# Performance work log

Measured on AMD Instinct MI355X. Metric: run time of the kernel, lower is better.

## Reference

```python
import jax, jax.numpy as jnp
import numpy as np

T, A = 10, 9           # input_dim_h, input_dim_w
HID = 128              # EncoderMLP hidden_dim default
D = 512                # n_latent_dims
G, K = 4, 32           # vqvae_groups, vqvae_n_embed
ACT_SCALE = 1.0


def setup_inputs() -> dict:
    key = jax.random.key(0)
    ks = jax.random.split(key, 16)
    N = 131072
    s = lambda k, shp, fan: jax.random.normal(k, shp, jnp.float32) * (1.0 / np.sqrt(fan))
    inp = {
        "state": jax.random.normal(ks[0], (N, T, A), jnp.float32),
        # encoder: (T*A)->128 relu, 128->128 relu, 128->512
        "enc_w1": s(ks[1], (T * A, HID), T * A), "enc_b1": jnp.zeros((HID,), jnp.float32),
        "enc_w2": s(ks[2], (HID, HID), HID),     "enc_b2": jnp.zeros((HID,), jnp.float32),
        "enc_w3": s(ks[3], (HID, D), HID),       "enc_b3": jnp.zeros((D,), jnp.float32),
        # decoder: 512->128 relu, 128->128 relu, 128->(T*A)
        "dec_w1": s(ks[4], (D, HID), D),         "dec_b1": jnp.zeros((HID,), jnp.float32),
        "dec_w2": s(ks[5], (HID, HID), HID),     "dec_b2": jnp.zeros((HID,), jnp.float32),
        "dec_w3": s(ks[6], (HID, T * A), HID),   "dec_b3": jnp.zeros((T * A,), jnp.float32),
        # residual VQ codebooks [G, K, D]
        "codebooks": jax.random.normal(ks[7], (G, K, D), jnp.float32),
    }
    return inp


def _mlp(x, w1, b1, w2, b2, w3, b3):
    h = jax.nn.relu(x @ w1 + b1)
    h = jax.nn.relu(h @ w2 + b2)
    return h @ w3 + b3


def reference(state, enc_w1, enc_b1, enc_w2, enc_b2, enc_w3, enc_b3,
              dec_w1, dec_b1, dec_w2, dec_b2, dec_w3, dec_b3, codebooks):
    N = state.shape[0]
    x = (state / ACT_SCALE).reshape(N, T * A)            # preprocess: 'N T A -> N (T A)'
    z = _mlp(x, enc_w1, enc_b1, enc_w2, enc_b2, enc_w3, enc_b3)  # [N, D]

    # Residual VQ over G quantizers (eval path): nearest-code per residual,
    # straight-through accumulation, per-quantizer commitment loss.
    residual = z
    quant = jnp.zeros_like(z)
    codes, losses = [], []
    for g in range(G):
        e = codebooks[g]                                  # [K, D]
        # ||r - e||^2 = ||r||^2 - 2 r.e + ||e||^2 ; ||r||^2 constant over K
        dist = jnp.sum(e * e, axis=-1)[None, :] - 2.0 * (residual @ e.T)  # [N, K]
        idx = jnp.argmin(dist, axis=-1)                   # [N]
        q = e[idx]                                        # [N, D] gather
        losses.append(jnp.mean((jax.lax.stop_gradient(q) - residual) ** 2))
        quant = quant + residual + jax.lax.stop_gradient(q - residual)  # straight-through
        residual = residual - jax.lax.stop_gradient(q)
        codes.append(idx)
    vq_code = jnp.stack(codes, axis=-1)                   # [N, G]
    vq_loss = jnp.sum(jnp.stack(losses))

    recon = _mlp(quant, dec_w1, dec_b1, dec_w2, dec_b2, dec_w3, dec_b3) * ACT_SCALE
    recon = recon.reshape(N, T, A)                        # 'N (T A) -> N T A'
    return quant, vq_code, recon, vq_loss
```

## Files before the change

kernel.cpp:

```cpp
#include <hip/hip_runtime.h>
#include <hip/hip_bf16.h>

#define NSAMP 131072
#define TA    90
#define HID   128
#define DLAT  512

#define OFF_CODE  67108864ll
#define OFF_RECON (67108864ll + 524288ll)
#define OFF_LOSS  (67108864ll + 524288ll + 11796480ll)

#define ACT_ST 68
#define WLF    8704
#define PZF    12800
#define SHF    13056
#define MSKF   8256
#define H2AF   8272
#define H2BF   8400
#define TAU    0.0625f

typedef __attribute__((ext_vector_type(8))) short bf16x8;
typedef __attribute__((ext_vector_type(4))) short s16x4;
typedef __attribute__((ext_vector_type(4))) float f32x4;
typedef unsigned short ushort_t;
#define MFMA16(a, b, c) __builtin_amdgcn_mfma_f32_16x16x32_bf16(a, b, c, 0, 0, 0)

__device__ __forceinline__ ushort_t f2bf(float f) {
    unsigned u = __float_as_uint(f);
    u = (u + 0x7FFF + ((u >> 16) & 1)) >> 16;
    return (ushort_t)u;
}
__device__ __forceinline__ float bf2f(ushort_t u) {
    return __uint_as_float(((unsigned)u) << 16);
}

__device__ __forceinline__ float dot512(const float* __restrict__ a,
                                        const float* __restrict__ b) {
    float s = 0.f;
    for (int i = 0; i < 128; ++i) {
        float4 x = ((const float4*)a)[i], y = ((const float4*)b)[i];
        s += x.x * y.x + x.y * y.y + x.z * y.z + x.w * y.w;
    }
    return s;
}

__device__ __forceinline__ void fma_tile(float (&acc)[8][4],
                                         const float* __restrict__ wl,
                                         const float* __restrict__ al) {
    float4 av = *(const float4*)al;
    float4 w0 = *(const float4*)wl;
    float4 w1 = *(const float4*)(wl + 4);
    float aa[4] = {av.x, av.y, av.z, av.w};
    float ww[8] = {w0.x, w0.y, w0.z, w0.w, w1.x, w1.y, w1.z, w1.w};
#pragma unroll
    for (int a = 0; a < 8; ++a)
#pragma unroll
        for (int b = 0; b < 4; ++b) acc[a][b] = fmaf(ww[a], aa[b], acc[a][b]);
}

__device__ __forceinline__ void gemm_dbuf(const float* __restrict__ w, int wstride,
                                          int inRows, int nch,
                                          const float* __restrict__ Act,
                                          float* __restrict__ Wl,
                                          float (&acc)[8][4],
                                          int t, int o0, int s0) {
    const int wr = t >> 4;
    const int wc = (t & 15) * 8;
    float4 c0, c1;
    {
        int r = wr < inRows ? wr : inRows - 1;
        const float* p = w + (size_t)r * wstride + wc;
        c0 = *(const float4*)p; c1 = *(const float4*)(p + 4);
    }
    *(float4*)&Wl[wr * 128 + wc] = c0;
    *(float4*)&Wl[wr * 128 + wc + 4] = c1;
    __syncthreads();
    for (int ch = 0; ch < nch; ++ch) {
        const float* Wc = &Wl[(ch & 1) * 2048];
        const bool more = (ch + 1 < nch);
        if (more) {
            int rr = (ch + 1) * 16 + wr;
            int r = rr < inRows ? rr : inRows - 1;
            const float* p = w + (size_t)r * wstride + wc;
            c0 = *(const float4*)p; c1 = *(const float4*)(p + 4);
        }
        const float* Ab = Act + (ch * 16) * ACT_ST + s0;
#pragma unroll
        for (int j = 0; j < 16; ++j)
            fma_tile(acc, &Wc[j * 128 + o0], Ab + j * ACT_ST);
        __syncthreads();
        if (more) {
            float* Wn = &Wl[((ch + 1) & 1) * 2048];
            *(float4*)&Wn[wr * 128 + wc] = c0;
            *(float4*)&Wn[wr * 128 + wc + 4] = c1;
            __syncthreads();
        }
    }
}

__global__ void k_prep(const float* __restrict__ cb, const float* __restrict__ w3,
                       const float* __restrict__ b3, const float* __restrict__ w1d,
                       const float* __restrict__ w2d, const float* __restrict__ w3d,
                       const float* __restrict__ w2e,
                       float* __restrict__ P, float* __restrict__ M,
                       float* __restrict__ t0, float* __restrict__ v,
                       float* __restrict__ csc, float* __restrict__ cbW,
                       ushort_t* __restrict__ Qbf, ushort_t* __restrict__ w2bf,
                       ushort_t* __restrict__ w3bf,
                       ushort_t* __restrict__ Mhibf, ushort_t* __restrict__ Mlobf,
                       ushort_t* __restrict__ w2ehi, ushort_t* __restrict__ w2elo) {
    int tbl = blockIdx.x >> 6;
    int gid = (blockIdx.x & 63) * 256 + threadIdx.x;
    int i = gid >> 7, j = gid & 127;
    if (tbl == 0) {
        P[gid] = dot512(cb + (size_t)i * 512, cb + (size_t)j * 512);
        if (gid < 128) t0[gid] = dot512(cb + (size_t)gid * 512, b3);
        if (gid == 0) csc[0] = dot512(b3, b3);
    } else if (tbl == 1) {
        M[gid] = dot512(w3 + (size_t)i * 512, cb + (size_t)j * 512);
    } else if (tbl == 2) {
        Qbf[gid] = f2bf(dot512(w3 + (size_t)i * 512, w3 + (size_t)j * 512));
        if (gid < 128) v[gid] = dot512(w3 + (size_t)gid * 512, b3);
    } else if (tbl == 3) {
        float s = 0.f;
        for (int d = 0; d < 512; ++d) s = fmaf(cb[(size_t)i * 512 + d], w1d[d * 128 + j], s);
        cbW[gid] = s;
    } else if (tbl == 4) {
        w2bf[gid] = f2bf(w2d[j * 128 + i]);
    } else if (tbl == 5) {
        if (gid < 96 * 128)
            w3bf[gid] = (i < 90) ? f2bf(w3d[j * TA + i]) : (ushort_t)0;
    } else if (tbl == 6) {
        float d = dot512(w3 + (size_t)j * 512, cb + (size_t)i * 512);
        ushort_t hi = f2bf(d);
        Mhibf[gid] = hi;
        Mlobf[gid] = f2bf(d - bf2f(hi));
    } else {
        float d = w2e[j * 128 + i];
        ushort_t hi = f2bf(d);
        w2ehi[gid] = hi;
        w2elo[gid] = f2bf(d - bf2f(hi));
    }
}

__launch_bounds__(256, 3)
__global__ void k_encvq(const float* __restrict__ X,
                        const float* __restrict__ w1, const float* __restrict__ b1,
                        const float* __restrict__ w2, const float* __restrict__ b2,
                        const ushort_t* __restrict__ w2ehi, const ushort_t* __restrict__ w2elo,
                        const float* __restrict__ Mt, const ushort_t* __restrict__ Qbf,
                        const ushort_t* __restrict__ Mhi, const ushort_t* __restrict__ Mlo,
                        const float* __restrict__ t0g, const float* __restrict__ vg,
                        const float* __restrict__ cg, const float* __restrict__ Pg,
                        float* __restrict__ codes_out, float* __restrict__ loss_acc) {
    __shared__ __align__(16) float SH[SHF];
    float* Act = SH;
    float* Wl  = SH + WLF;
    ushort_t* hAhi = (ushort_t*)SH;
    ushort_t* hAlo = (ushort_t*)(SH + 4096);
    const int t = threadIdx.x;
    const int st = t & 15, ct = t >> 4;
    const int s0 = st * 4, o0 = ct * 8;
    const int row0 = blockIdx.x * 64;

    float rb1[8];
#pragma unroll
    for (int i = 0; i < 8; ++i) rb1[i] = b1[o0 + i];

    for (int it = 0; it < 24; ++it) {
        int idx = it * 256 + t;
        int j = idx >> 6, s = idx & 63;
        Act[j * ACT_ST + s] = (j < 90) ? X[(size_t)(row0 + s) * TA + j] : 0.f;
    }

    float acc[8][4];
#pragma unroll
    for (int a = 0; a < 8; ++a)
#pragma unroll
        for (int b = 0; b < 4; ++b) acc[a][b] = 0.f;
    gemm_dbuf(w1, HID, 90, 6, Act, Wl, acc, t, o0, s0);

    {
#pragma unroll
        for (int b = 0; b < 4; ++b) {
            int s = s0 + b;
            bf16x8 pkh, pkl;
#pragma unroll
            for (int a = 0; a < 8; ++a) {
                float hv = fmaxf(acc[a][b] + rb1[a], 0.f);
                acc[a][b] = hv;
                ushort_t hi = f2bf(hv);
                pkh[a] = (short)hi;
                pkl[a] = (short)f2bf(hv - bf2f(hi));
            }
            int adr = ((s << 7) + o0) ^ ((s & 7) << 3);
            *(bf16x8*)&hAhi[adr] = pkh;
            *(bf16x8*)&hAlo[adr] = pkl;
        }
    }
    __syncthreads();

    const int wv = t >> 6, lane = t & 63, lr = lane & 15, lg = lane >> 4;

    {
        f32x4 c2[2][4];
#pragma unroll
        for (int m = 0; m < 2; ++m)
#pragma unroll
            for (int n = 0; n < 4; ++n) c2[m][n] = (f32x4){0.f, 0.f, 0.f, 0.f};
#pragma unroll
        for (int kt = 0; kt < 4; ++kt) {
            bf16x8 ah[2], al[2], bhi[4], blo[4];
#pragma unroll
            for (int m = 0; m < 2; ++m) {
                int arow = (32 * wv + 16 * m + lr) * 128 + kt * 32 + lg * 8;
                ah[m] = *(const bf16x8*)&w2ehi[arow];
                al[m] = *(const bf16x8*)&w2elo[arow];
            }
#pragma unroll
            for (int n = 0; n < 4; ++n) {
                int s = 16 * n + lr;
                int adr = ((s << 7) + kt * 32 + lg * 8) ^ ((s & 7) << 3);
                bhi[n] = *(const bf16x8*)&hAhi[adr];
                blo[n] = *(const bf16x8*)&hAlo[adr];
            }
#pragma unroll
            for (int m = 0; m < 2; ++m)
#pragma unroll
                for (int n = 0; n < 4; ++n) {
                    c2[m][n] = MFMA16(ah[m], bhi[n], c2[m][n]);
                    c2[m][n] = MFMA16(ah[m], blo[n], c2[m][n]);
                    c2[m][n] = MFMA16(al[m], bhi[n], c2[m][n]);
                }
        }
        __syncthreads();
        float rbf[2][4];
#pragma unroll
        for (int m = 0; m < 2; ++m)
#pragma unroll
            for (int r = 0; r < 4; ++r) rbf[m][r] = b2[32 * wv + 16 * m + lg * 4 + r];
#pragma unroll
        for (int m = 0; m < 2; ++m)
#pragma unroll
            for (int n = 0; n < 4; ++n) {
                int s = 16 * n + lr;
                s16x4 ph, pl;
#pragma unroll
                for (int r = 0; r < 4; ++r) {
                    float hv = fmaxf(c2[m][n][r] + rbf[m][r], 0.f);
                    ushort_t hi = f2bf(hv);
                    ph[r] = (short)hi;
                    pl[r] = (short)f2bf(hv - bf2f(hi));
                }
                int ob2 = 32 * wv + 16 * m + lg * 4;
                int adr = ((s << 7) + ob2) ^ ((s & 7) << 3);
                *(s16x4*)&hAhi[adr] = ph;
                *(s16x4*)&hAlo[adr] = pl;
            }
    }
    __syncthreads();

    f32x4 sc[2][4];
    {
        f32x4 qc[2][4];
#pragma unroll
        for (int m = 0; m < 2; ++m)
#pragma unroll
            for (int n = 0; n < 4; ++n) {
                qc[m][n] = (f32x4){0.f, 0.f, 0.f, 0.f};
                sc[m][n] = (f32x4){0.f, 0.f, 0.f, 0.f};
            }
#pragma unroll
        for (int kt = 0; kt < 4; ++kt) {
            bf16x8 aq[2], amh[2], aml[2], bhi[4], blo[4];
#pragma unroll
            for (int m = 0; m < 2; ++m) {
                int arow = (32 * wv + 16 * m + lr) * 128 + kt * 32 + lg * 8;
                aq[m]  = *(const bf16x8*)&Qbf[arow];
                amh[m] = *(const bf16x8*)&Mhi[arow];
                aml[m] = *(const bf16x8*)&Mlo[arow];
            }
#pragma unroll
            for (int n = 0; n < 4; ++n) {
                int s = 16 * n + lr;
                int adr = ((s << 7) + kt * 32 + lg * 8) ^ ((s & 7) << 3);
                bhi[n] = *(const bf16x8*)&hAhi[adr];
                blo[n] = *(const bf16x8*)&hAlo[adr];
            }
#pragma unroll
            for (int m = 0; m < 2; ++m)
#pragma unroll
                for (int n = 0; n < 4; ++n) {
                    qc[m][n] = MFMA16(aq[m], bhi[n], qc[m][n]);
                    sc[m][n] = MFMA16(amh[m], bhi[n], sc[m][n]);
                    sc[m][n] = MFMA16(amh[m], blo[n], sc[m][n]);
                    sc[m][n] = MFMA16(aml[m], bhi[n], sc[m][n]);
                }
        }
        float v2[2][4];
#pragma unroll
        for (int m = 0; m < 2; ++m)
#pragma unroll
            for (int r = 0; r < 4; ++r) v2[m][r] = 2.f * vg[32 * wv + 16 * m + lg * 4 + r];
#pragma unroll
        for (int n = 0; n < 4; ++n) {
            int s = 16 * n + lr;
            float p = 0.f;
#pragma unroll
            for (int m = 0; m < 2; ++m)
#pragma unroll
                for (int r = 0; r < 4; ++r) {
                    int o = 32 * wv + 16 * m + lg * 4 + r;
                    int adr = ((s << 7) + o) ^ ((s & 7) << 3);
                    float hv = bf2f(hAhi[adr]) + bf2f(hAlo[adr]);
                    p = fmaf(qc[m][n][r] + v2[m][r], hv, p);
                }
            p += __shfl_xor(p, 16);
            p += __shfl_xor(p, 32);
            if (lg == 0) SH[PZF + wv * 64 + s] = p;
        }
    }
    __syncthreads();

#pragma unroll
    for (int m = 0; m < 2; ++m)
#pragma unroll
        for (int n = 0; n < 4; ++n) {
            int s = 16 * n + lr;
#pragma unroll
            for (int r = 0; r < 4; ++r) {
                int o = 32 * wv + 16 * m + lg * 4 + r;
                SH[s * 129 + o] = sc[m][n][r] + t0g[o];
            }
        }
    __syncthreads();

    int cs[4];
    if (t < 64) {
        float marg = 3.4e38f;
#pragma unroll
        for (int g = 0; g < 4; ++g) {
            float best = 3.4e38f, best2 = 3.4e38f; int bi = g * 32;
#pragma unroll
            for (int k = 0; k < 32; ++k) {
                int c = g * 32 + k;
                float zd = SH[t * 129 + c];
                float nr = Pg[c * 128 + c];
                float a2 = 0.f;
#pragma unroll
                for (int gp = 0; gp < g; ++gp) a2 += Pg[cs[gp] * 128 + c];
                float dist = nr - 2.f * (zd - a2);
                if (dist < best) { best2 = best; best = dist; bi = c; }
                else if (dist < best2) { best2 = dist; }
            }
            cs[g] = bi;
            float m2 = best2 - best;
            marg = (m2 < marg) ? m2 : marg;
        }
        unsigned long long mk = __ballot(marg < TAU);
        if (t == 0) *(unsigned long long*)&SH[MSKF] = mk;
    }
    __syncthreads();

    const unsigned long long mask = *(const unsigned long long*)&SH[MSKF];

    {
        unsigned long long mk = mask;
        while (mk) {
            int nA = (int)__ffsll((long long)mk) - 1; mk &= mk - 1;
            int nB = -1;
            if (mk) { nB = (int)__ffsll((long long)mk) - 1; mk &= mk - 1; }
            if ((t & 15) == (nA >> 2)) {
                int bb = nA & 3;
                if (bb == 0) {
#pragma unroll
                    for (int a = 0; a < 8; ++a) SH[H2AF + o0 + a] = acc[a][0];
                } else if (bb == 1) {
#pragma unroll
                    for (int a = 0; a < 8; ++a) SH[H2AF + o0 + a] = acc[a][1];
                } else if (bb == 2) {
#pragma unroll
                    for (int a = 0; a < 8; ++a) SH[H2AF + o0 + a] = acc[a][2];
                } else {
#pragma unroll
                    for (int a = 0; a < 8; ++a) SH[H2AF + o0 + a] = acc[a][3];
                }
            }
            if (nB >= 0 && (t & 15) == (nB >> 2)) {
                int bb = nB & 3;
                if (bb == 0) {
#pragma unroll
                    for (int a = 0; a < 8; ++a) SH[H2BF + o0 + a] = acc[a][0];
                } else if (bb == 1) {
#pragma unroll
                    for (int a = 0; a < 8; ++a) SH[H2BF + o0 + a] = acc[a][1];
                } else if (bb == 2) {
#pragma unroll
                    for (int a = 0; a < 8; ++a) SH[H2BF + o0 + a] = acc[a][2];
                } else {
#pragma unroll
                    for (int a = 0; a < 8; ++a) SH[H2BF + o0 + a] = acc[a][3];
                }
            }
            __syncthreads();
            int grp = t >> 7, tt = t & 127;
            int s2 = grp ? nB : nA;
            float hv2 = 0.f;
            if (s2 >= 0) {
                const float* h1c = &SH[grp ? H2BF : H2AF];
                for (int j = 0; j < 128; ++j)
                    hv2 = fmaf(h1c[j], w2[(size_t)j * 128 + tt], hv2);
                hv2 = fmaxf(hv2 + b2[tt], 0.f);
            }
            __syncthreads();
            if (s2 >= 0) SH[(grp ? H2BF : H2AF) + tt] = hv2;
            __syncthreads();
            if (s2 >= 0) {
                const float* h2c = &SH[grp ? H2BF : H2AF];
                float a = 0.f;
                for (int j = 0; j < 128; ++j)
                    a = fmaf(h2c[j], Mt[(size_t)j * 128 + tt], a);
                SH[s2 * 129 + tt] = a + t0g[tt];
            }
            __syncthreads();
        }
    }

    if (t < 64 && ((mask >> t) & 1ull)) {
#pragma unroll
        for (int g = 0; g < 4; ++g) {
            float best = 3.4e38f; int bi = g * 32;
#pragma unroll
            for (int k = 0; k < 32; ++k) {
                int c = g * 32 + k;
                float zd = SH[t * 129 + c];
                float nr = Pg[c * 128 + c];
                float a2 = 0.f;
#pragma unroll
                for (int gp = 0; gp < g; ++gp) a2 += Pg[cs[gp] * 128 + c];
                float dist = nr - 2.f * (zd - a2);
                if (dist < best) { best = dist; bi = c; }
            }
            cs[g] = bi;
        }
    }

    if (t < 64) {
        float znorm = cg[0] + SH[PZF + t] + SH[PZF + 64 + t]
                    + SH[PZF + 128 + t] + SH[PZF + 192 + t];
        float S1 = 0.f, Sp = 0.f, msum = 0.f;
#pragma unroll
        for (int g = 0; g < 4; ++g) {
            int c = cs[g];
            float zd = SH[t * 129 + c];
            float nr = Pg[c * 128 + c];
            float a2 = 0.f;
#pragma unroll
            for (int gp = 0; gp < g; ++gp) a2 += Pg[cs[gp] * 128 + c];
            S1 += zd;
            Sp += nr + 2.f * a2;
            msum += (znorm - 2.f * S1 + Sp);
            codes_out[(size_t)(row0 + t) * 4 + g] = (float)(c - g * 32);
        }
#pragma unroll
        for (int off = 32; off; off >>= 1) msum += __shfl_down(msum, off);
        if (t == 0) atomicAdd(&loss_acc[0], msum);
    }
}

__launch_bounds__(256, 4)
__global__ void k_dec(const float* __restrict__ codes_f, const float* __restrict__ cb,
                      const float* __restrict__ cbW, const float* __restrict__ b1,
                      const ushort_t* __restrict__ w2bf, const float* __restrict__ b2,
                      const ushort_t* __restrict__ w3bf, const float* __restrict__ b3,
                      float* __restrict__ quant_out, float* __restrict__ recon_out) {
    __shared__ __align__(16) unsigned char SHB[39424];
    int* cods = (int*)SHB;
    ushort_t* h2bf = (ushort_t*)SHB;
    ushort_t* h1bf = (ushort_t*)(SHB + 16384);
    float* Rl = (float*)(SHB + 16384);
    const int t = threadIdx.x;
    const int st = t & 15, ct = t >> 4;
    const int s0 = st * 4, o0 = ct * 8;
    const int row0 = blockIdx.x * 64;

    cods[t] = ((t & 3) << 5) + (int)codes_f[(size_t)row0 * 4 + t];
    float rb1[8];
#pragma unroll
    for (int i = 0; i < 8; ++i) rb1[i] = b1[o0 + i];
    __syncthreads();

    for (int i = 0; i < 32; ++i) {
        int idx4 = i * 256 + t;
        int s = idx4 >> 7, d4 = (idx4 & 127) * 4;
        const int* cp = &cods[s * 4];
        float4 a = *(const float4*)&cb[(size_t)cp[0] * 512 + d4];
        float4 b = *(const float4*)&cb[(size_t)cp[1] * 512 + d4];
        float4 c = *(const float4*)&cb[(size_t)cp[2] * 512 + d4];
        float4 d = *(const float4*)&cb[(size_t)cp[3] * 512 + d4];
        float4 vv;
        vv.x = a.x + b.x + c.x + d.x;
        vv.y = a.y + b.y + c.y + d.y;
        vv.z = a.z + b.z + c.z + d.z;
        vv.w = a.w + b.w + c.w + d.w;
        *(float4*)&quant_out[(size_t)(row0 + s) * 512 + d4] = vv;
    }

    {
        float accL[8][4];
#pragma unroll
        for (int b = 0; b < 4; ++b) {
            const int* cp = &cods[(s0 + b) * 4];
            float u[8] = {0, 0, 0, 0, 0, 0, 0, 0};
#pragma unroll
            for (int g = 0; g < 4; ++g) {
                const float* r = &cbW[(size_t)cp[g] * 128 + o0];
                float4 x0 = *(const float4*)r, x1 = *(const float4*)(r + 4);
                u[0] += x0.x; u[1] += x0.y; u[2] += x0.z; u[3] += x0.w;
                u[4] += x1.x; u[5] += x1.y; u[6] += x1.z; u[7] += x1.w;
            }
#pragma unroll
            for (int a = 0; a < 8; ++a) accL[a][b] = u[a];
        }
#pragma unroll
        for (int b = 0; b < 4; ++b) {
            int s = s0 + b;
            bf16x8 pk;
#pragma unroll
            for (int a = 0; a < 8; ++a)
                pk[a] = (short)f2bf(fmaxf(accL[a][b] + rb1[a], 0.f));
            *(bf16x8*)&h1bf[((s << 7) + o0) ^ ((s & 7) << 3)] = pk;
        }
    }
    __syncthreads();

    const int wv = t >> 6, lane = t & 63, lr = lane & 15, lg = lane >> 4;

    {
        f32x4 c2[2][4];
#pragma unroll
        for (int m = 0; m < 2; ++m)
#pragma unroll
            for (int n = 0; n < 4; ++n) c2[m][n] = (f32x4){0.f, 0.f, 0.f, 0.f};
#pragma unroll
        for (int kt = 0; kt < 4; ++kt) {
            bf16x8 af[2], bfr[4];
#pragma unroll
            for (int m = 0; m < 2; ++m)
                af[m] = *(const bf16x8*)&w2bf[(32 * wv + 16 * m + lr) * 128 + kt * 32 + lg * 8];
#pragma unroll
            for (int n = 0; n < 4; ++n) {
                int s = 16 * n + lr;
                bfr[n] = *(const bf16x8*)&h1bf[((s << 7) + kt * 32 + lg * 8) ^ ((s & 7) << 3)];
            }
#pragma unroll
            for (int m = 0; m < 2; ++m)
#pragma unroll
                for (int n = 0; n < 4; ++n)
                    c2[m][n] = MFMA16(af[m], bfr[n], c2[m][n]);
        }
        float rb[2][4];
#pragma unroll
        for (int m = 0; m < 2; ++m)
#pragma unroll
            for (int r = 0; r < 4; ++r) rb[m][r] = b2[32 * wv + 16 * m + lg * 4 + r];
#pragma unroll
        for (int m = 0; m < 2; ++m)
#pragma unroll
            for (int n = 0; n < 4; ++n) {
                int s = 16 * n + lr;
                s16x4 pk;
#pragma unroll
                for (int r = 0; r < 4; ++r)
                    pk[r] = (short)f2bf(fmaxf(c2[m][n][r] + rb[m][r], 0.f));
                int ob2 = 32 * wv + 16 * m + lg * 4;
                *(s16x4*)&h2bf[((s << 7) + ob2) ^ ((s & 7) << 3)] = pk;
            }
    }
    __syncthreads();

    {
        f32x4 c3[6];
#pragma unroll
        for (int m = 0; m < 6; ++m) c3[m] = (f32x4){0.f, 0.f, 0.f, 0.f};
        const int sB = 16 * wv + lr;
#pragma unroll
        for (int kt = 0; kt < 4; ++kt) {
            bf16x8 bfr = *(const bf16x8*)&h2bf[((sB << 7) + kt * 32 + lg * 8) ^ ((sB & 7) << 3)];
#pragma unroll
            for (int mt = 0; mt < 6; ++mt) {
                bf16x8 af = *(const bf16x8*)&w3bf[(16 * mt + lr) * 128 + kt * 32 + lg * 8];
                c3[mt] = MFMA16(af, bfr, c3[mt]);
            }
        }
#pragma unroll
        for (int mt = 0; mt < 6; ++mt)
#pragma unroll
            for (int r = 0; r < 4; ++r) {
                int o = 16 * mt + lg * 4 + r;
                if (o < 90) Rl[sB * 90 + o] = c3[mt][r] + b3[o];
            }
    }
    __syncthreads();

    {
        const float4* R4v = (const float4*)Rl;
        float4* G4 = (float4*)(recon_out + (size_t)row0 * 90);
#pragma unroll
        for (int it = 0; it < 6; ++it) {
            int i4 = it * 256 + t;
            if (i4 < 1440) G4[i4] = R4v[i4];
        }
    }
}

__global__ void k_loss(const float* __restrict__ acc, float* __restrict__ out) {
    out[0] = acc[0] * (1.0f / ((float)NSAMP * (float)DLAT));
}

extern "C" void kernel_launch(void* const* d_in, const int* in_sizes, int n_in,
                              void* d_out, int out_size, void* d_ws, size_t ws_size,
                              hipStream_t stream) {
    const float* state  = (const float*)d_in[0];
    const float* enc_w1 = (const float*)d_in[1];
    const float* enc_b1 = (const float*)d_in[2];
    const float* enc_w2 = (const float*)d_in[3];
    const float* enc_b2 = (const float*)d_in[4];
    const float* enc_w3 = (const float*)d_in[5];
    const float* enc_b3 = (const float*)d_in[6];
    const float* dec_w1 = (const float*)d_in[7];
    const float* dec_b1 = (const float*)d_in[8];
    const float* dec_w2 = (const float*)d_in[9];
    const float* dec_b2 = (const float*)d_in[10];
    const float* dec_w3 = (const float*)d_in[11];
    const float* dec_b3 = (const float*)d_in[12];
    const float* cb     = (const float*)d_in[13];

    float* out = (float*)d_out;
    float* P   = out;
    float* M   = out + 16384;
    ushort_t* Mhi = (ushort_t*)(out + 32768);
    ushort_t* Mlo = (ushort_t*)(out + 40960);
    float* t0  = out + 49152;
    float* v   = out + 49280;
    float* csc = out + 49408;
    ushort_t* w2ehi = (ushort_t*)(out + 49664);
    ushort_t* w2elo = (ushort_t*)(out + 57856);
    float* ws = (float*)d_ws;
    float* loss_acc = ws;
    float* cbW = ws + 256;
    ushort_t* Qbf  = (ushort_t*)(ws + 16640);
    ushort_t* w2bf = (ushort_t*)(ws + 24832);
    ushort_t* w3bf = (ushort_t*)(ws + 33024);

    hipMemsetAsync(d_ws, 0, 16, stream);
    k_prep<<<512, 256, 0, stream>>>(cb, enc_w3, enc_b3, dec_w1, dec_w2, dec_w3,
                                    enc_w2,
                                    P, M, t0, v, csc, cbW, Qbf, w2bf, w3bf,
                                    Mhi, Mlo, w2ehi, w2elo);
    k_encvq<<<NSAMP / 64, 256, 0, stream>>>(state, enc_w1, enc_b1, enc_w2, enc_b2,
                                            w2ehi, w2elo,
                                            M, Qbf, Mhi, Mlo, t0, v, csc, P,
                                            out + OFF_CODE, loss_acc);
    k_dec<<<NSAMP / 64, 256, 0, stream>>>(out + OFF_CODE, cb, cbW,
                                          dec_b1, w2bf, dec_b2, w3bf, dec_b3,
                                          out, out + OFF_RECON);
    k_loss<<<1, 1, 0, stream>>>(loss_acc, out + OFF_LOSS);
}
```

Baseline: 348.4 us.

## Move encoder layer 1 to split-bf16 MFMA and recompute near-tie rows from global

```diff
diff --git a/kernel.cpp b/kernel.cpp
--- a/kernel.cpp
+++ b/kernel.cpp
@@ -10,14 +10,12 @@
 #define OFF_RECON (67108864ll + 524288ll)
 #define OFF_LOSS  (67108864ll + 524288ll + 11796480ll)
 
-#define ACT_ST 68
-#define WLF    8704
-#define PZF    12800
-#define SHF    13056
+#define PZF    8704
+#define SHF    8960
 #define MSKF   8256
 #define H2AF   8272
 #define H2BF   8400
-#define TAU    0.0625f
+#define TAU    0.08f
 
 typedef __attribute__((ext_vector_type(8))) short bf16x8;
 typedef __attribute__((ext_vector_type(4))) short s16x4;
@@ -44,71 +42,18 @@
     return s;
 }
 
-__device__ __forceinline__ void fma_tile(float (&acc)[8][4],
-                                         const float* __restrict__ wl,
-                                         const float* __restrict__ al) {
-    float4 av = *(const float4*)al;
-    float4 w0 = *(const float4*)wl;
-    float4 w1 = *(const float4*)(wl + 4);
-    float aa[4] = {av.x, av.y, av.z, av.w};
-    float ww[8] = {w0.x, w0.y, w0.z, w0.w, w1.x, w1.y, w1.z, w1.w};
-#pragma unroll
-    for (int a = 0; a < 8; ++a)
-#pragma unroll
-        for (int b = 0; b < 4; ++b) acc[a][b] = fmaf(ww[a], aa[b], acc[a][b]);
-}
-
-__device__ __forceinline__ void gemm_dbuf(const float* __restrict__ w, int wstride,
-                                          int inRows, int nch,
-                                          const float* __restrict__ Act,
-                                          float* __restrict__ Wl,
-                                          float (&acc)[8][4],
-                                          int t, int o0, int s0) {
-    const int wr = t >> 4;
-    const int wc = (t & 15) * 8;
-    float4 c0, c1;
-    {
-        int r = wr < inRows ? wr : inRows - 1;
-        const float* p = w + (size_t)r * wstride + wc;
-        c0 = *(const float4*)p; c1 = *(const float4*)(p + 4);
-    }
-    *(float4*)&Wl[wr * 128 + wc] = c0;
-    *(float4*)&Wl[wr * 128 + wc + 4] = c1;
-    __syncthreads();
-    for (int ch = 0; ch < nch; ++ch) {
-        const float* Wc = &Wl[(ch & 1) * 2048];
-        const bool more = (ch + 1 < nch);
-        if (more) {
-            int rr = (ch + 1) * 16 + wr;
-            int r = rr < inRows ? rr : inRows - 1;
-            const float* p = w + (size_t)r * wstride + wc;
-            c0 = *(const float4*)p; c1 = *(const float4*)(p + 4);
-        }
-        const float* Ab = Act + (ch * 16) * ACT_ST + s0;
-#pragma unroll
-        for (int j = 0; j < 16; ++j)
-            fma_tile(acc, &Wc[j * 128 + o0], Ab + j * ACT_ST);
-        __syncthreads();
-        if (more) {
-            float* Wn = &Wl[((ch + 1) & 1) * 2048];
-            *(float4*)&Wn[wr * 128 + wc] = c0;
-            *(float4*)&Wn[wr * 128 + wc + 4] = c1;
-            __syncthreads();
-        }
-    }
-}
-
 __global__ void k_prep(const float* __restrict__ cb, const float* __restrict__ w3,
                        const float* __restrict__ b3, const float* __restrict__ w1d,
                        const float* __restrict__ w2d, const float* __restrict__ w3d,
-                       const float* __restrict__ w2e,
+                       const float* __restrict__ w2e, const float* __restrict__ w1e,
                        float* __restrict__ P, float* __restrict__ M,
                        float* __restrict__ t0, float* __restrict__ v,
                        float* __restrict__ csc, float* __restrict__ cbW,
                        ushort_t* __restrict__ Qbf, ushort_t* __restrict__ w2bf,
                        ushort_t* __restrict__ w3bf,
                        ushort_t* __restrict__ Mhibf, ushort_t* __restrict__ Mlobf,
-                       ushort_t* __restrict__ w2ehi, ushort_t* __restrict__ w2elo) {
+                       ushort_t* __restrict__ w2ehi, ushort_t* __restrict__ w2elo,
+                       ushort_t* __restrict__ w1ehi, ushort_t* __restrict__ w1elo) {
     int tbl = blockIdx.x >> 6;
     int gid = (blockIdx.x & 63) * 256 + threadIdx.x;
     int i = gid >> 7, j = gid & 127;
@@ -135,18 +80,24 @@
         ushort_t hi = f2bf(d);
         Mhibf[gid] = hi;
         Mlobf[gid] = f2bf(d - bf2f(hi));
-    } else {
+    } else if (tbl == 7) {
         float d = w2e[j * 128 + i];
         ushort_t hi = f2bf(d);
         w2ehi[gid] = hi;
         w2elo[gid] = f2bf(d - bf2f(hi));
-    }
-}
-
-__launch_bounds__(256, 3)
+    } else {
+        float d = (j < 90) ? w1e[(size_t)j * 128 + i] : 0.f;
+        ushort_t hi = f2bf(d);
+        w1ehi[gid] = hi;
+        w1elo[gid] = f2bf(d - bf2f(hi));
+    }
+}
+
+__launch_bounds__(256, 4)
 __global__ void k_encvq(const float* __restrict__ X,
                         const float* __restrict__ w1, const float* __restrict__ b1,
                         const float* __restrict__ w2, const float* __restrict__ b2,
+                        const ushort_t* __restrict__ w1ehi, const ushort_t* __restrict__ w1elo,
                         const ushort_t* __restrict__ w2ehi, const ushort_t* __restrict__ w2elo,
                         const float* __restrict__ Mt, const ushort_t* __restrict__ Qbf,
                         const ushort_t* __restrict__ Mhi, const ushort_t* __restrict__ Mlo,
@@ -154,53 +105,80 @@
                         const float* __restrict__ cg, const float* __restrict__ Pg,
                         float* __restrict__ codes_out, float* __restrict__ loss_acc) {
     __shared__ __align__(16) float SH[SHF];
-    float* Act = SH;
-    float* Wl  = SH + WLF;
-    ushort_t* hAhi = (ushort_t*)SH;
-    ushort_t* hAlo = (ushort_t*)(SH + 4096);
+    ushort_t* sphi = (ushort_t*)SH;
+    ushort_t* splo = (ushort_t*)(SH + 4096);
     const int t = threadIdx.x;
-    const int st = t & 15, ct = t >> 4;
-    const int s0 = st * 4, o0 = ct * 8;
     const int row0 = blockIdx.x * 64;
-
-    float rb1[8];
-#pragma unroll
-    for (int i = 0; i < 8; ++i) rb1[i] = b1[o0 + i];
+    const int wv = t >> 6, lane = t & 63, lr = lane & 15, lg = lane >> 4;
 
     for (int it = 0; it < 24; ++it) {
         int idx = it * 256 + t;
-        int j = idx >> 6, s = idx & 63;
-        Act[j * ACT_ST + s] = (j < 90) ? X[(size_t)(row0 + s) * TA + j] : 0.f;
-    }
-
-    float acc[8][4];
-#pragma unroll
-    for (int a = 0; a < 8; ++a)
-#pragma unroll
-        for (int b = 0; b < 4; ++b) acc[a][b] = 0.f;
-    gemm_dbuf(w1, HID, 90, 6, Act, Wl, acc, t, o0, s0);
-
-    {
-#pragma unroll
-        for (int b = 0; b < 4; ++b) {
-            int s = s0 + b;
-            bf16x8 pkh, pkl;
-#pragma unroll
-            for (int a = 0; a < 8; ++a) {
-                float hv = fmaxf(acc[a][b] + rb1[a], 0.f);
-                acc[a][b] = hv;
-                ushort_t hi = f2bf(hv);
-                pkh[a] = (short)hi;
-                pkl[a] = (short)f2bf(hv - bf2f(hi));
-            }
-            int adr = ((s << 7) + o0) ^ ((s & 7) << 3);
-            *(bf16x8*)&hAhi[adr] = pkh;
-            *(bf16x8*)&hAlo[adr] = pkl;
-        }
-    }
-    __syncthreads();
-
-    const int wv = t >> 6, lane = t & 63, lr = lane & 15, lg = lane >> 4;
+        int s = idx / 96, j = idx - 96 * s;
+        float xv = (j < 90) ? X[(size_t)(row0 + s) * TA + j] : 0.f;
+        ushort_t hi = f2bf(xv);
+        int adr = ((s << 7) + j) ^ ((s & 7) << 3);
+        sphi[adr] = hi;
+        splo[adr] = f2bf(xv - bf2f(hi));
+    }
+    __syncthreads();
+
+    {
+        f32x4 c1[2][4];
+#pragma unroll
+        for (int m = 0; m < 2; ++m)
+#pragma unroll
+            for (int n = 0; n < 4; ++n) c1[m][n] = (f32x4){0.f, 0.f, 0.f, 0.f};
+#pragma unroll
+        for (int kt = 0; kt < 3; ++kt) {
+            bf16x8 ah[2], al[2], bhi[4], blo[4];
+#pragma unroll
+            for (int m = 0; m < 2; ++m) {
+                int arow = (32 * wv + 16 * m + lr) * 128 + kt * 32 + lg * 8;
+                ah[m] = *(const bf16x8*)&w1ehi[arow];
+                al[m] = *(const bf16x8*)&w1elo[arow];
+            }
+#pragma unroll
+            for (int n = 0; n < 4; ++n) {
+                int s = 16 * n + lr;
+                int adr = ((s << 7) + kt * 32 + lg * 8) ^ ((s & 7) << 3);
+                bhi[n] = *(const bf16x8*)&sphi[adr];
+                blo[n] = *(const bf16x8*)&splo[adr];
+            }
+#pragma unroll
+            for (int m = 0; m < 2; ++m)
+#pragma unroll
+                for (int n = 0; n < 4; ++n) {
+                    c1[m][n] = MFMA16(ah[m], bhi[n], c1[m][n]);
+                    c1[m][n] = MFMA16(ah[m], blo[n], c1[m][n]);
+                    c1[m][n] = MFMA16(al[m], bhi[n], c1[m][n]);
+                }
+        }
+        __syncthreads();
+        float rbf[2][4];
+#pragma unroll
+        for (int m = 0; m < 2; ++m)
+#pragma unroll
+            for (int r = 0; r < 4; ++r) rbf[m][r] = b1[32 * wv + 16 * m + lg * 4 + r];
+#pragma unroll
+        for (int m = 0; m < 2; ++m)
+#pragma unroll
+            for (int n = 0; n < 4; ++n) {
+                int s = 16 * n + lr;
+                s16x4 ph, pl;
+#pragma unroll
+                for (int r = 0; r < 4; ++r) {
+                    float hv = fmaxf(c1[m][n][r] + rbf[m][r], 0.f);
+                    ushort_t hi = f2bf(hv);
+                    ph[r] = (short)hi;
+                    pl[r] = (short)f2bf(hv - bf2f(hi));
+                }
+                int ob2 = 32 * wv + 16 * m + lg * 4;
+                int adr = ((s << 7) + ob2) ^ ((s & 7) << 3);
+                *(s16x4*)&sphi[adr] = ph;
+                *(s16x4*)&splo[adr] = pl;
+            }
+    }
+    __syncthreads();
 
     {
         f32x4 c2[2][4];
@@ -221,8 +199,8 @@
             for (int n = 0; n < 4; ++n) {
                 int s = 16 * n + lr;
                 int adr = ((s << 7) + kt * 32 + lg * 8) ^ ((s & 7) << 3);
-                bhi[n] = *(const bf16x8*)&hAhi[adr];
-                blo[n] = *(const bf16x8*)&hAlo[adr];
+                bhi[n] = *(const bf16x8*)&sphi[adr];
+                blo[n] = *(const bf16x8*)&splo[adr];
             }
 #pragma unroll
             for (int m = 0; m < 2; ++m)
@@ -254,8 +232,8 @@
                 }
                 int ob2 = 32 * wv + 16 * m + lg * 4;
                 int adr = ((s << 7) + ob2) ^ ((s & 7) << 3);
-                *(s16x4*)&hAhi[adr] = ph;
-                *(s16x4*)&hAlo[adr] = pl;
+                *(s16x4*)&sphi[adr] = ph;
+                *(s16x4*)&splo[adr] = pl;
             }
     }
     __syncthreads();
@@ -284,8 +262,8 @@
             for (int n = 0; n < 4; ++n) {
                 int s = 16 * n + lr;
                 int adr = ((s << 7) + kt * 32 + lg * 8) ^ ((s & 7) << 3);
-                bhi[n] = *(const bf16x8*)&hAhi[adr];
-                blo[n] = *(const bf16x8*)&hAlo[adr];
+                bhi[n] = *(const bf16x8*)&sphi[adr];
+                blo[n] = *(const bf16x8*)&splo[adr];
             }
 #pragma unroll
             for (int m = 0; m < 2; ++m)
@@ -312,7 +290,7 @@
                 for (int r = 0; r < 4; ++r) {
                     int o = 32 * wv + 16 * m + lg * 4 + r;
                     int adr = ((s << 7) + o) ^ ((s & 7) << 3);
-                    float hv = bf2f(hAhi[adr]) + bf2f(hAlo[adr]);
+                    float hv = bf2f(sphi[adr]) + bf2f(splo[adr]);
                     p = fmaf(qc[m][n][r] + v2[m][r], hv, p);
                 }
             p += __shfl_xor(p, 16);
@@ -370,41 +348,17 @@
             int nA = (int)__ffsll((long long)mk) - 1; mk &= mk - 1;
             int nB = -1;
             if (mk) { nB = (int)__ffsll((long long)mk) - 1; mk &= mk - 1; }
-            if ((t & 15) == (nA >> 2)) {
-                int bb = nA & 3;
-                if (bb == 0) {
-#pragma unroll
-                    for (int a = 0; a < 8; ++a) SH[H2AF + o0 + a] = acc[a][0];
-                } else if (bb == 1) {
-#pragma unroll
-                    for (int a = 0; a < 8; ++a) SH[H2AF + o0 + a] = acc[a][1];
-                } else if (bb == 2) {
-#pragma unroll
-                    for (int a = 0; a < 8; ++a) SH[H2AF + o0 + a] = acc[a][2];
-                } else {
-#pragma unroll
-                    for (int a = 0; a < 8; ++a) SH[H2AF + o0 + a] = acc[a][3];
-                }
-            }
-            if (nB >= 0 && (t & 15) == (nB >> 2)) {
-                int bb = nB & 3;
-                if (bb == 0) {
-#pragma unroll
-                    for (int a = 0; a < 8; ++a) SH[H2BF + o0 + a] = acc[a][0];
-                } else if (bb == 1) {
-#pragma unroll
-                    for (int a = 0; a < 8; ++a) SH[H2BF + o0 + a] = acc[a][1];
-                } else if (bb == 2) {
-#pragma unroll
-                    for (int a = 0; a < 8; ++a) SH[H2BF + o0 + a] = acc[a][2];
-                } else {
-#pragma unroll
-                    for (int a = 0; a < 8; ++a) SH[H2BF + o0 + a] = acc[a][3];
-                }
-            }
-            __syncthreads();
             int grp = t >> 7, tt = t & 127;
             int s2 = grp ? nB : nA;
+            float hv1 = 0.f;
+            if (s2 >= 0) {
+                const float* xr = X + (size_t)(row0 + s2) * TA;
+                for (int j = 0; j < 90; ++j)
+                    hv1 = fmaf(xr[j], w1[j * 128 + tt], hv1);
+                hv1 = fmaxf(hv1 + b1[tt], 0.f);
+                SH[(grp ? H2BF : H2AF) + tt] = hv1;
+            }
+            __syncthreads();
             float hv2 = 0.f;
             if (s2 >= 0) {
                 const float* h1c = &SH[grp ? H2BF : H2AF];
@@ -646,6 +600,8 @@
     float* csc = out + 49408;
     ushort_t* w2ehi = (ushort_t*)(out + 49664);
     ushort_t* w2elo = (ushort_t*)(out + 57856);
+    ushort_t* w1ehi = (ushort_t*)(out + 66048);
+    ushort_t* w1elo = (ushort_t*)(out + 74240);
     float* ws = (float*)d_ws;
     float* loss_acc = ws;
     float* cbW = ws + 256;
@@ -654,12 +610,12 @@
     ushort_t* w3bf = (ushort_t*)(ws + 33024);
 
     hipMemsetAsync(d_ws, 0, 16, stream);
-    k_prep<<<512, 256, 0, stream>>>(cb, enc_w3, enc_b3, dec_w1, dec_w2, dec_w3,
-                                    enc_w2,
+    k_prep<<<576, 256, 0, stream>>>(cb, enc_w3, enc_b3, dec_w1, dec_w2, dec_w3,
+                                    enc_w2, enc_w1,
                                     P, M, t0, v, csc, cbW, Qbf, w2bf, w3bf,
-                                    Mhi, Mlo, w2ehi, w2elo);
+                                    Mhi, Mlo, w2ehi, w2elo, w1ehi, w1elo);
     k_encvq<<<NSAMP / 64, 256, 0, stream>>>(state, enc_w1, enc_b1, enc_w2, enc_b2,
-                                            w2ehi, w2elo,
+                                            w1ehi, w1elo, w2ehi, w2elo,
                                             M, Qbf, Mhi, Mlo, t0, v, csc, P,
                                             out + OFF_CODE, loss_acc);
     k_dec<<<NSAMP / 64, 256, 0, stream>>>(out + OFF_CODE, cb, cbW,
```

New measurement: 352.3 us. No clear change (+1.1%).
